# Kernel optimization log

Hardware: AMD Instinct MI355X
Metric: run time of the kernel (lower is better)

Reference implementation:

```python
import jax, jax.numpy as jnp
import numpy as np

B, S, E = 2, 2048, 2048
H, KVH, D = 16, 4, 128
GROUPS = H // KVH
WINDOW = 1024
CAP = 50.0
ROPE_BASE = 10000.0
RMS_EPS = 1e-6
LN_EPS = 1e-5

def setup_inputs() -> dict:
    key = jax.random.key(0)
    ks = jax.random.split(key, 5)
    return {
        "x": jax.random.normal(ks[0], (B, S, E), jnp.float32),
        "Wq": jax.random.normal(ks[1], (E, E), jnp.float32) * (1.0 / np.sqrt(E)),
        "Wk": jax.random.normal(ks[2], (KVH * D, E), jnp.float32) * (1.0 / np.sqrt(E)),
        "Wv": jax.random.normal(ks[3], (KVH * D, E), jnp.float32) * (1.0 / np.sqrt(E)),
        "Wo": jax.random.normal(ks[4], (E, E), jnp.float32) * (1.0 / np.sqrt(E * H)),
        "q_norm_w": jnp.ones((D,), jnp.float32),
        "k_norm_w": jnp.ones((D,), jnp.float32),
        "ln_gamma": jnp.ones((E,), jnp.float32),
        "ln_beta": jnp.zeros((E,), jnp.float32),
    }

def _rmsnorm(t, w):
    # normalize over last (head) dim
    var = jnp.mean(jnp.square(t), axis=-1, keepdims=True)
    return t * jax.lax.rsqrt(var + RMS_EPS) * w

def _rope(t):
    # t: [B, h, S, D]; rotate-half RoPE
    half = D // 2
    inv_freq = 1.0 / (ROPE_BASE ** (jnp.arange(0, D, 2, dtype=jnp.float32) / D))  # [D/2]
    ang = jnp.arange(S, dtype=jnp.float32)[:, None] * inv_freq[None, :]  # [S, D/2]
    cos = jnp.concatenate([jnp.cos(ang), jnp.cos(ang)], axis=-1)  # [S, D]
    sin = jnp.concatenate([jnp.sin(ang), jnp.sin(ang)], axis=-1)
    t1, t2 = t[..., :half], t[..., half:]
    rot = jnp.concatenate([-t2, t1], axis=-1)
    return t * cos + rot * sin

def reference(x, Wq, Wk, Wv, Wo, q_norm_w, k_norm_w, ln_gamma, ln_beta):
    b, s, _ = x.shape
    q = (x @ Wq.T).reshape(b, s, H, D).transpose(0, 2, 1, 3)    # [B,H,S,D]
    k = (x @ Wk.T).reshape(b, s, KVH, D).transpose(0, 2, 1, 3)  # [B,KVH,S,D]
    v = (x @ Wv.T).reshape(b, s, KVH, D).transpose(0, 2, 1, 3)
    # QK-RMSNorm (Gemma/PaLM2 style), then RoPE
    q = _rope(_rmsnorm(q, q_norm_w))
    k = _rope(_rmsnorm(k, k_norm_w))
    # GQA: repeat KV heads to match query heads
    k = jnp.repeat(k, GROUPS, axis=1)  # [B,H,S,D]
    v = jnp.repeat(v, GROUPS, axis=1)
    scores = jnp.einsum('bhqd,bhkd->bhqk', q, k) / jnp.sqrt(jnp.asarray(D, x.dtype))
    # tanh logit softcap (Gemma2)
    scores = CAP * jnp.tanh(scores / CAP)
    # causal + sliding-window mask: attend to j with 0 <= i-j < WINDOW
    i = jnp.arange(s)[:, None]
    j = jnp.arange(s)[None, :]
    mask = (j <= i) & ((i - j) < WINDOW)  # [S,S]
    neg = jnp.finfo(scores.dtype).min
    scores = jnp.where(mask[None, None], scores, neg)
    attn = jax.nn.softmax(scores, axis=-1)
    out = jnp.einsum('bhqk,bhkd->bhqd', attn, v)  # [B,H,S,D]
    out = out.transpose(0, 2, 1, 3).reshape(b, s, E) @ Wo.T
    # residual + LayerNorm (post-norm)
    y = x + out
    mu = jnp.mean(y, axis=-1, keepdims=True)
    var = jnp.var(y, axis=-1, keepdims=True)
    return (y - mu) * jax.lax.rsqrt(var + LN_EPS) * ln_gamma + ln_beta
```

## Files before the change

kernel.cpp:

```cpp
#include <hip/hip_runtime.h>
#include <stdint.h>

typedef __attribute__((ext_vector_type(8))) short short8;
typedef __attribute__((ext_vector_type(4))) float f32x4;
typedef unsigned short u16;
typedef unsigned int u32;

#define NTOK 4096
#define E 2048
#define S 2048
#define NH 16
#define NKVH 4
#define HD 128
#define NQKV 3072

__device__ __forceinline__ float bf2f(u16 u) {
    return __uint_as_float(((u32)u) << 16);
}
__device__ __forceinline__ u16 f2bf(float f) {
    u32 u = __float_as_uint(f);
    u32 r = (u + 0x7fffu + ((u >> 16) & 1u)) >> 16;
    return (u16)r;
}
__device__ __forceinline__ void gload_lds16(const u16* g, u16* l) {
    __builtin_amdgcn_global_load_lds(
        (const __attribute__((address_space(1))) unsigned int*)(g),
        (__attribute__((address_space(3))) unsigned int*)(l), 16, 0, 0);
}

__global__ void cast5(const float* __restrict__ x, const float* __restrict__ wq,
                      const float* __restrict__ wk, const float* __restrict__ wv,
                      const float* __restrict__ wo,
                      u16* __restrict__ xb, u16* __restrict__ wqkvb,
                      u16* __restrict__ wob) {
    int i = blockIdx.x * 256 + threadIdx.x;
    const float* s; u16* d; int rel;
    if (i < 2097152)      { s = x;  d = xb;  rel = i; }
    else if (i < 3145728) { s = wq; d = wqkvb; rel = i - 2097152; }
    else if (i < 3407872) { s = wk; d = wqkvb + 4194304; rel = i - 3145728; }
    else if (i < 3670016) { s = wv; d = wqkvb + 5242880; rel = i - 3407872; }
    else                  { s = wo; d = wob; rel = i - 3670016; }
    float4 v = *(const float4*)(s + (size_t)rel * 4);
    ushort4 o;
    o.x = f2bf(v.x); o.y = f2bf(v.y); o.z = f2bf(v.z); o.w = f2bf(v.w);
    *(ushort4*)(d + (size_t)rel * 4) = o;
}

#define LADDR(row, ko) ((row) * 64 + ((ko) ^ (((row) & 7) << 3)))
#define GSB   __builtin_amdgcn_sched_barrier(0)
#define GBAR  __builtin_amdgcn_s_barrier()
#define LGKM0 do { asm volatile("s_waitcnt lgkmcnt(0)" ::: "memory"); GSB; } while (0)
#define MIDBAR do { GSB; GBAR; LGKM0; } while (0)
#define ENDBAR do { __builtin_amdgcn_s_setprio(0); GSB; GBAR; } while (0)

__device__ __forceinline__ void stage1(u16* lds, const u16* g, int row0,
                                       int kt, int K, int tid) {
    const int rr = tid >> 3;
    const int chunk = (tid & 7) ^ (rr & 7);
    gload_lds16(g + (size_t)(row0 + rr) * K + kt + chunk * 8,
                lds + (row0 + (tid >> 6) * 8) * 64);
}

__global__ __launch_bounds__(512, 2)
void gemm_qkv(const u16* __restrict__ A, const u16* __restrict__ Bt,
              float* __restrict__ C, int M, int N, int K) {
    __shared__ u16 As2[2 * 8192];
    __shared__ u16 Bs2[2 * 24576];
    const int tid = threadIdx.x;
    const int w = tid >> 6, lane = tid & 63;
    const int lr = lane & 15, quad = lane >> 4;
    const int qo = quad * 8;
    const int wr = w >> 2, wc = w & 3;
    const int am = wr * 64;
    const int bn = wc * 96;

    const int nbx = N / 384;
    int wg = blockIdx.x;
    {
        const int nwg = gridDim.x;
        const int q = nwg >> 3, r = nwg & 7;
        const int xcd = wg & 7, loc = wg >> 3;
        wg = (xcd < r ? xcd * (q + 1) : r * (q + 1) + (xcd - r) * q) + loc;
    }
    const int n0 = (wg % nbx) * 384;
    const int m0 = (wg / nbx) * 128;

    const u16* gA = A + (size_t)m0 * K;
    const u16* gB = Bt + (size_t)n0 * K;
    const int nt = K >> 6;

    f32x4 acc[4][6];
#pragma unroll
    for (int mi = 0; mi < 4; mi++)
#pragma unroll
        for (int ni = 0; ni < 6; ni++)
            acc[mi][ni] = (f32x4){0.f, 0.f, 0.f, 0.f};

    short8 af[4][2], bf[6][2];

    stage1(As2, gA, 0, 0, K, tid);
    stage1(As2, gA, 64, 0, K, tid);
#pragma unroll
    for (int r = 0; r < 6; r++) stage1(Bs2, gB, r * 64, 0, K, tid);
    if (nt > 1) {
        stage1(As2 + 8192, gA, 0, 64, K, tid);
        stage1(As2 + 8192, gA, 64, 64, K, tid);
#pragma unroll
        for (int r = 0; r < 4; r++) stage1(Bs2 + 24576, gB, r * 64, 64, K, tid);
        asm volatile("s_waitcnt vmcnt(6)" ::: "memory");
    } else {
        asm volatile("s_waitcnt vmcnt(0)" ::: "memory");
    }
    GSB; GBAR;

    for (int t = 0; t < nt; ++t) {
        const int pb = t & 1;
        u16* Ap = As2 + pb * 8192;
        u16* Bp = Bs2 + pb * 24576;
        u16* Bn = Bs2 + (pb ^ 1) * 24576;
        const int kt1 = (t + 1) << 6, kt2 = (t + 2) << 6;

#pragma unroll
        for (int mi = 0; mi < 4; mi++)
#pragma unroll
            for (int kk = 0; kk < 2; kk++)
                af[mi][kk] = *(const short8*)&Ap[LADDR(am + mi * 16 + lr, kk * 32 + qo)];
#pragma unroll
        for (int ni = 0; ni < 3; ni++)
#pragma unroll
            for (int kk = 0; kk < 2; kk++)
                bf[ni][kk] = *(const short8*)&Bp[LADDR(bn + ni * 16 + lr, kk * 32 + qo)];
        if (t + 1 < nt) {
            stage1(Bn, gB, 256, kt1, K, tid);
            stage1(Bn, gB, 320, kt1, K, tid);
        }
        MIDBAR;
        __builtin_amdgcn_s_setprio(1);
#pragma unroll
        for (int mi = 0; mi < 2; mi++)
#pragma unroll
            for (int ni = 0; ni < 3; ni++)
#pragma unroll
                for (int kk = 0; kk < 2; kk++)
                    acc[mi][ni] = __builtin_amdgcn_mfma_f32_16x16x32_bf16(
                        af[mi][kk], bf[ni][kk], acc[mi][ni], 0, 0, 0);
        ENDBAR;

#pragma unroll
        for (int ni = 3; ni < 6; ni++)
#pragma unroll
            for (int kk = 0; kk < 2; kk++)
                bf[ni][kk] = *(const short8*)&Bp[LADDR(bn + ni * 16 + lr, kk * 32 + qo)];
        if (t + 2 < nt) {
            stage1(Ap, gA, 0, kt2, K, tid);
            stage1(Ap, gA, 64, kt2, K, tid);
        }
        MIDBAR;
        __builtin_amdgcn_s_setprio(1);
#pragma unroll
        for (int mi = 0; mi < 2; mi++)
#pragma unroll
            for (int ni = 3; ni < 6; ni++)
#pragma unroll
                for (int kk = 0; kk < 2; kk++)
                    acc[mi][ni] = __builtin_amdgcn_mfma_f32_16x16x32_bf16(
                        af[mi][kk], bf[ni][kk], acc[mi][ni], 0, 0, 0);
        ENDBAR;

        if (t + 2 < nt) {
#pragma unroll
            for (int r = 0; r < 4; r++) stage1(Bp, gB, r * 64, kt2, K, tid);
        }
        __builtin_amdgcn_s_setprio(1);
#pragma unroll
        for (int mi = 2; mi < 4; mi++)
#pragma unroll
            for (int ni = 0; ni < 6; ni++)
#pragma unroll
                for (int kk = 0; kk < 2; kk++)
                    acc[mi][ni] = __builtin_amdgcn_mfma_f32_16x16x32_bf16(
                        af[mi][kk], bf[ni][kk], acc[mi][ni], 0, 0, 0);
        __builtin_amdgcn_s_setprio(0);
        if (t + 2 >= nt) {
            asm volatile("s_waitcnt vmcnt(0)" ::: "memory");
        } else {
            asm volatile("s_waitcnt vmcnt(6)" ::: "memory");
        }
        GSB; GBAR;
    }

#pragma unroll
    for (int mi = 0; mi < 4; mi++)
#pragma unroll
        for (int ni = 0; ni < 6; ni++) {
            const int row = m0 + am + mi * 16 + quad * 4;
            const int col = n0 + bn + ni * 16 + lr;
            f32x4 v = acc[mi][ni];
            C[(size_t)(row + 0) * N + col] = v[0];
            C[(size_t)(row + 1) * N + col] = v[1];
            C[(size_t)(row + 2) * N + col] = v[2];
            C[(size_t)(row + 3) * N + col] = v[3];
        }
}

__device__ __forceinline__ void stageA(u16* lds, const u16* g, int ldsrow0,
                                       int g0, int g1, int kt, int K, int tid) {
    const int rr = tid >> 3;
    const int chunk = (tid & 7) ^ (rr & 7);
    const int w8 = (tid >> 6) * 8;
    gload_lds16(g + (size_t)(g0 + rr) * K + kt + chunk * 8,
                lds + (ldsrow0 + w8) * 64);
    gload_lds16(g + (size_t)(g1 + rr) * K + kt + chunk * 8,
                lds + (ldsrow0 + 64 + w8) * 64);
}
__device__ __forceinline__ void stageB(u16* lds, const u16* g, int ldsrow0,
                                       int b0, int b1, int kt, int K, int tid) {
    const int rr = tid >> 3;
    const int grow = (rr & 31) | ((rr & 32) << 1);
    const int chunk = (tid & 7) ^ (rr & 7);
    const int w8 = (tid >> 6) * 8;
    gload_lds16(g + (size_t)(b0 + grow) * K + kt + chunk * 8,
                lds + (ldsrow0 + w8) * 64);
    gload_lds16(g + (size_t)(b1 + grow) * K + kt + chunk * 8,
                lds + (ldsrow0 + 64 + w8) * 64);
}

__global__ __launch_bounds__(512, 2)
void gemm8p(const u16* __restrict__ A, const u16* __restrict__ Bt,
            float* __restrict__ C, int M, int N, int K, int ksz, int nsplit) {
    __shared__ u16 As[2 * 16384];
    __shared__ u16 Bs[2 * 16384];
    const int tid = threadIdx.x;
    const int w = tid >> 6, lane = tid & 63;
    const int lr = lane & 15, quad = lane >> 4;
    const int qo = quad * 8;
    const int wm = (w >> 2) * 128, wn = (w & 3) * 64;
    const int wmh = (w >> 2) * 64, wnq = (w & 3) * 32;

    const int nbx = N >> 8;
    int wg = blockIdx.x;
    {
        const int nwg = gridDim.x;
        const int q = nwg >> 3, r = nwg & 7;
        const int xcd = wg & 7, loc = wg >> 3;
        wg = (xcd < r ? xcd * (q + 1) : r * (q + 1) + (xcd - r) * q) + loc;
    }
    int split = 0;
    if (nsplit == 2) { split = wg & 1; wg >>= 1; }
    const int n0 = (wg % nbx) << 8;
    const int m0 = (wg / nbx) << 8;

    const u16* gA = A + (size_t)m0 * K + split * ksz;
    const u16* gB = Bt + (size_t)n0 * K + split * ksz;
    C += (size_t)split * M * N;
    const int nt = ksz >> 6;

    f32x4 acc[8][4];
#pragma unroll
    for (int mi = 0; mi < 8; mi++)
#pragma unroll
        for (int ni = 0; ni < 4; ni++)
            acc[mi][ni] = (f32x4){0.f, 0.f, 0.f, 0.f};

    short8 alo[4][2], ahi[4][2], blo[2][2], bhi[2][2];

    stageA(As, gA, 0, 0, 128, 0, K, tid);
    stageB(Bs, gB, 0, 0, 128, 0, K, tid);
    stageB(Bs, gB, 128, 32, 160, 0, K, tid);
    stageA(As, gA, 128, 64, 192, 0, K, tid);
    if (nt > 1) {
        stageA(As + 16384, gA, 0, 0, 128, 64, K, tid);
        stageB(Bs + 16384, gB, 0, 0, 128, 64, K, tid);
        stageB(Bs + 16384, gB, 128, 32, 160, 64, K, tid);
        asm volatile("s_waitcnt vmcnt(6)" ::: "memory");
    } else {
        asm volatile("s_waitcnt vmcnt(0)" ::: "memory");
    }
    GSB; GBAR;

    for (int t = 0; t < nt; ++t) {
        const int pb = t & 1;
        u16* Ap = As + pb * 16384;
        u16* Bp = Bs + pb * 16384;
        u16* An = As + (pb ^ 1) * 16384;
        const int kt1 = (t + 1) << 6, kt2 = (t + 2) << 6;

#pragma unroll
        for (int mi = 0; mi < 4; mi++)
#pragma unroll
            for (int kk = 0; kk < 2; kk++)
                alo[mi][kk] = *(const short8*)&Ap[LADDR(wmh + mi * 16 + lr, kk * 32 + qo)];
#pragma unroll
        for (int ni = 0; ni < 2; ni++)
#pragma unroll
            for (int kk = 0; kk < 2; kk++)
                blo[ni][kk] = *(const short8*)&Bp[LADDR(wnq + ni * 16 + lr, kk * 32 + qo)];
        if (t + 1 < nt) stageA(An, gA, 128, 64, 192, kt1, K, tid);
        MIDBAR;
        __builtin_amdgcn_s_setprio(1);
#pragma unroll
        for (int mi = 0; mi < 4; mi++)
#pragma unroll
            for (int ni = 0; ni < 2; ni++)
#pragma unroll
                for (int kk = 0; kk < 2; kk++)
                    acc[mi][ni] = __builtin_amdgcn_mfma_f32_16x16x32_bf16(
                        alo[mi][kk], blo[ni][kk], acc[mi][ni], 0, 0, 0);
        ENDBAR;

#pragma unroll
        for (int ni = 0; ni < 2; ni++)
#pragma unroll
            for (int kk = 0; kk < 2; kk++)
                bhi[ni][kk] = *(const short8*)&Bp[LADDR(128 + wnq + ni * 16 + lr, kk * 32 + qo)];
        if (t + 2 < nt) stageA(Ap, gA, 0, 0, 128, kt2, K, tid);
        MIDBAR;
        __builtin_amdgcn_s_setprio(1);
#pragma unroll
        for (int mi = 0; mi < 4; mi++)
#pragma unroll
            for (int ni = 0; ni < 2; ni++)
#pragma unroll
                for (int kk = 0; kk < 2; kk++)
                    acc[mi][ni + 2] = __builtin_amdgcn_mfma_f32_16x16x32_bf16(
                        alo[mi][kk], bhi[ni][kk], acc[mi][ni + 2], 0, 0, 0);
        ENDBAR;

#pragma unroll
        for (int mi = 0; mi < 4; mi++)
#pragma unroll
            for (int kk = 0; kk < 2; kk++)
                ahi[mi][kk] = *(const short8*)&Ap[LADDR(128 + wmh + mi * 16 + lr, kk * 32 + qo)];
        if (t + 2 < nt) stageB(Bp, gB, 0, 0, 128, kt2, K, tid);
        MIDBAR;
        __builtin_amdgcn_s_setprio(1);
#pragma unroll
        for (int mi = 0; mi < 4; mi++)
#pragma unroll
            for (int ni = 0; ni < 2; ni++)
#pragma unroll
                for (int kk = 0; kk < 2; kk++)
                    acc[mi + 4][ni + 2] = __builtin_amdgcn_mfma_f32_16x16x32_bf16(
                        ahi[mi][kk], bhi[ni][kk], acc[mi + 4][ni + 2], 0, 0, 0);
        ENDBAR;

        if (t + 2 < nt) stageB(Bp, gB, 128, 32, 160, kt2, K, tid);
        __builtin_amdgcn_s_setprio(1);
#pragma unroll
        for (int mi = 0; mi < 4; mi++)
#pragma unroll
            for (int ni = 0; ni < 2; ni++)
#pragma unroll
                for (int kk = 0; kk < 2; kk++)
                    acc[mi + 4][ni] = __builtin_amdgcn_mfma_f32_16x16x32_bf16(
                        ahi[mi][kk], blo[ni][kk], acc[mi + 4][ni], 0, 0, 0);
        __builtin_amdgcn_s_setprio(0);
        if (t + 2 >= nt) {
            asm volatile("s_waitcnt vmcnt(0)" ::: "memory");
        } else {
            asm volatile("s_waitcnt vmcnt(6)" ::: "memory");
        }
        GSB; GBAR;
    }

#pragma unroll
    for (int mi = 0; mi < 8; mi++)
#pragma unroll
        for (int ni = 0; ni < 4; ni++) {
            const int row = m0 + wm + mi * 16 + quad * 4;
            const int col = n0 + wn + ni * 16 + lr;
            f32x4 v = acc[mi][ni];
            C[(size_t)(row + 0) * N + col] = v[0];
            C[(size_t)(row + 1) * N + col] = v[1];
            C[(size_t)(row + 2) * N + col] = v[2];
            C[(size_t)(row + 3) * N + col] = v[3];
        }
}

#define LDT 65
#define RMSBLKS 20480
__global__ __launch_bounds__(256)
void prep(const float* __restrict__ qkv,
          const float* __restrict__ qw, const float* __restrict__ kw,
          u16* __restrict__ qdst, u16* __restrict__ kdst, u16* __restrict__ vdst) {
    __shared__ u16 Ts[128 * LDT];
    if (blockIdx.x < RMSBLKS) {
        int p = blockIdx.x * 4 + (threadIdx.x >> 6);
        int lane = threadIdx.x & 63;
        const float* src; const float* w; u16* dst; int HH;
        if (p < NTOK * NH) { src = qkv; w = qw; dst = qdst; HH = NH; }
        else { p -= NTOK * NH; src = qkv + 2048; w = kw; dst = kdst; HH = NKVH; }
        int n = p / HH;
        int h = p - n * HH;
        int b = n >> 11;
        int s = n & 2047;
        const float* row = src + (size_t)n * NQKV + h * HD;
        float t1 = row[lane];
        float t2 = row[lane + 64];
        float ss = t1 * t1 + t2 * t2;
#pragma unroll
        for (int o = 1; o < 64; o <<= 1) ss += __shfl_xor(ss, o);
        float r = rsqrtf(ss * (1.f / 128.f) + 1e-6f);
        float a1 = t1 * r * w[lane];
        float a2 = t2 * r * w[lane + 64];
        float freq = expf(lane * -0.14391156831212787f);
        float ang = (float)s * freq;
        float sn, cs;
        sincosf(ang, &sn, &cs);
        float o1 = a1 * cs - a2 * sn;
        float o2 = a2 * cs + a1 * sn;
        size_t base = (((size_t)(b * HH + h)) * S + s) * HD;
        dst[base + lane] = f2bf(o1);
        dst[base + 64 + lane] = f2bf(o2);
    } else {
        const int idx = blockIdx.x - RMSBLKS;
        const int t = threadIdx.x;
        const int s0 = (idx & 31) * 64;
        const int kh = (idx >> 5) & 3;
        const int b = idx >> 7;
        const float* base = qkv + ((size_t)(b * S + s0)) * NQKV + 2560 + kh * HD;
#pragma unroll
        for (int i = 0; i < 8; i++) {
            int ii = i * 256 + t;
            int r = ii >> 5, c4 = (ii & 31) * 4;
            float4 v = *(const float4*)(base + (size_t)r * NQKV + c4);
            Ts[(c4 + 0) * LDT + r] = f2bf(v.x);
            Ts[(c4 + 1) * LDT + r] = f2bf(v.y);
            Ts[(c4 + 2) * LDT + r] = f2bf(v.z);
            Ts[(c4 + 3) * LDT + r] = f2bf(v.w);
        }
        __syncthreads();
        u16* obase = vdst + ((size_t)(b * NKVH + kh) * HD) * S + s0;
#pragma unroll
        for (int i = 0; i < 4; i++) {
            int ii = i * 256 + t;
            int d = ii >> 3, s8 = (ii & 7) * 8;
            const u16* row = &Ts[d * LDT + s8];
            short8 o;
#pragma unroll
            for (int j = 0; j < 8; j++) o[j] = (short)row[j];
            *(short8*)(obase + (size_t)d * S + s8) = o;
        }
    }
}

#define KSX(key, cb) ((key) * 128 + ((((cb) ^ ((key) & 15))) * 8))
#define VSX(d, cb)   ((d) * 64 + ((((cb) ^ ((d) & 7))) * 8))
#define PSX(row, cb) ((row) * 64 + ((((cb) ^ ((row) & 7))) * 8))
#define QBLK 64

__global__ __launch_bounds__(256, 4)
void attn_mfma(const u16* __restrict__ qa, const u16* __restrict__ ka,
               const u16* __restrict__ vt, u16* __restrict__ out) {
    __shared__ u16 Ks[64 * 128];
    __shared__ u16 Vs[128 * 64];
    __shared__ u16 Ps[64 * 64];
    const int tid = threadIdx.x;
    const int w = tid >> 6, lane = tid & 63;
    const int lr = lane & 15, quad = lane >> 4;

    const int bid = blockIdx.x;
    const int g = bid >> 8, p = bid & 255;
    const int j = p >> 5, hb = p & 31;
    int qt;
    if (g == 0) qt = 31 - j;
    else if (g == 1) qt = 23 - j;
    else if (g == 2) qt = 8 + j;
    else qt = 7 - j;
    const int h = hb >> 1, b = hb & 1;
    const int kh = h >> 2;
    const int q0 = qt * QBLK;
    const int qg0 = q0 + w * 16;

    const float KQK = 0.0051006974f;
    const float KP  = -144.26950408889634f;

    const u16* kbase0 = ka + (((size_t)(b * NKVH + kh)) * S) * HD;
    const u16* vtbase0 = vt + ((size_t)(b * NKVH + kh) * HD) * S;

    short8 qf[4];
    {
        const u16* qrow = qa + (((size_t)(b * NH + h)) * S + qg0 + lr) * HD;
#pragma unroll
        for (int c = 0; c < 4; c++)
            qf[c] = *(const short8*)(qrow + c * 32 + quad * 8);
    }

    f32x4 O[8];
#pragma unroll
    for (int dt = 0; dt < 8; dt++) O[dt] = (f32x4){0.f, 0.f, 0.f, 0.f};
    float l[4] = {0.f, 0.f, 0.f, 0.f};

    const int jt0 = (q0 >= 1024) ? (q0 - 1024) : 0;
    const int jtend = q0;
    const int qmin = qg0, qmax = qg0 + 15;

    for (int jt = jt0; jt <= jtend; jt += 64) {
        const u16* kbase = kbase0 + (size_t)jt * HD;
        const u16* vtbase = vtbase0 + jt;
        __syncthreads();
#pragma unroll
        for (int i = 0; i < 4; i++) {
            int idx = i * 256 + tid;
            int key = idx >> 4, cbk = (idx & 15) ^ (key & 15);
            gload_lds16(kbase + (size_t)key * HD + cbk * 8,
                        &Ks[(i * 256 + w * 64) * 8]);
            int dd = idx >> 3, cbv = (idx & 7) ^ (dd & 7);
            gload_lds16(vtbase + (size_t)dd * S + cbv * 8,
                        &Vs[(i * 256 + w * 64) * 8]);
        }
        __syncthreads();

        u16* Pw = &Ps[w * 16 * 64];
        bool any = false;

#pragma unroll
        for (int kt = 0; kt < 4; kt++) {
            const int keymin = jt + kt * 16;
            bool need = (keymin <= qmax) && (keymin + 15 >= qmin - 1023);
            bool full = (keymin + 15 <= qmin) && (keymin >= qmax - 1023);
            if (need) {
                any = true;
                f32x4 a = (f32x4){0.f, 0.f, 0.f, 0.f};
                __builtin_amdgcn_s_setprio(1);
#pragma unroll
                for (int c = 0; c < 4; c++) {
                    short8 kf = *(const short8*)(&Ks[KSX(kt * 16 + lr, 4 * c + quad)]);
                    a = __builtin_amdgcn_mfma_f32_16x16x32_bf16(qf[c], kf, a, 0, 0, 0);
                }
                __builtin_amdgcn_s_setprio(0);
#pragma unroll
                for (int r = 0; r < 4; r++) {
                    float t = __builtin_amdgcn_exp2f(a[r] * KQK);
                    float p2 = __builtin_amdgcn_exp2f(
                        KP * __builtin_amdgcn_rcpf(t + 1.f));
                    if (!full) {
                        int rel = keymin + lr - (qg0 + quad * 4 + r);
                        bool valid = (rel <= 0) && (rel > -1024);
                        p2 = valid ? p2 : 0.f;
                    }
                    l[r] += p2;
                    Pw[PSX(quad * 4 + r, kt * 2 + (lr >> 3)) + (lr & 7)] =
                        (u16)(__float_as_uint(p2) >> 16);
                }
            } else {
#pragma unroll
                for (int r = 0; r < 4; r++)
                    Pw[PSX(quad * 4 + r, kt * 2 + (lr >> 3)) + (lr & 7)] = 0;
            }
        }

        if (any) {
            __builtin_amdgcn_s_setprio(1);
#pragma unroll
            for (int c2 = 0; c2 < 2; c2++) {
                short8 pf = *(const short8*)(&Pw[PSX(lr, c2 * 4 + quad)]);
#pragma unroll
                for (int dt = 0; dt < 8; dt++) {
                    short8 vf = *(const short8*)(&Vs[VSX(dt * 16 + lr, c2 * 4 + quad)]);
                    O[dt] = __builtin_amdgcn_mfma_f32_16x16x32_bf16(pf, vf, O[dt], 0, 0, 0);
                }
            }
            __builtin_amdgcn_s_setprio(0);
        }
    }

#pragma unroll
    for (int r = 0; r < 4; r++) {
        l[r] += __shfl_xor(l[r], 1);
        l[r] += __shfl_xor(l[r], 2);
        l[r] += __shfl_xor(l[r], 4);
        l[r] += __shfl_xor(l[r], 8);
    }
#pragma unroll
    for (int r = 0; r < 4; r++) {
        float inv = 1.f / l[r];
        u16* orow = out + ((size_t)(b * S + qg0 + quad * 4 + r)) * E + h * HD;
#pragma unroll
        for (int dt = 0; dt < 8; dt++)
            orow[dt * 16 + lr] = f2bf(O[dt][r] * inv);
    }
}

__global__ __launch_bounds__(256)
void ln_kernel(const float* __restrict__ x, const float* __restrict__ pr,
               const float* __restrict__ pr2,
               const float* __restrict__ g, const float* __restrict__ be,
               float* __restrict__ out) {
    int n = blockIdx.x;
    int tid = threadIdx.x;
    const float* xr = x + (size_t)n * E;
    const float* p = pr + (size_t)n * E;
    const float* p2 = pr2 + (size_t)n * E;
    float y[8];
    float s = 0.f, ss = 0.f;
#pragma unroll
    for (int i = 0; i < 2; i++) {
        float4 a = *(const float4*)(xr + tid * 8 + i * 4);
        float4 b = *(const float4*)(p + tid * 8 + i * 4);
        float4 cc = *(const float4*)(p2 + tid * 8 + i * 4);
        float v0 = a.x + b.x + cc.x, v1 = a.y + b.y + cc.y;
        float v2 = a.z + b.z + cc.z, v3 = a.w + b.w + cc.w;
        y[i * 4 + 0] = v0; y[i * 4 + 1] = v1; y[i * 4 + 2] = v2; y[i * 4 + 3] = v3;
        s += v0 + v1 + v2 + v3;
        ss += v0 * v0 + v1 * v1 + v2 * v2 + v3 * v3;
    }
#pragma unroll
    for (int o = 1; o < 64; o <<= 1) {
        s += __shfl_xor(s, o);
        ss += __shfl_xor(ss, o);
    }
    __shared__ float r0[4], r1[4];
    int w = tid >> 6;
    if ((tid & 63) == 0) { r0[w] = s; r1[w] = ss; }
    __syncthreads();
    s = r0[0] + r0[1] + r0[2] + r0[3];
    ss = r1[0] + r1[1] + r1[2] + r1[3];
    float mu = s * (1.f / 2048.f);
    float var = ss * (1.f / 2048.f) - mu * mu;
    float rs = rsqrtf(var + 1e-5f);
    float* orow = out + (size_t)n * E;
#pragma unroll
    for (int i = 0; i < 8; i++) {
        int c = tid * 8 + i;
        orow[c] = (y[i] - mu) * rs * g[c] + be[c];
    }
}

extern "C" void kernel_launch(void* const* d_in, const int* in_sizes, int n_in,
                              void* d_out, int out_size, void* d_ws, size_t ws_size,
                              hipStream_t stream) {
    (void)in_sizes; (void)n_in; (void)out_size; (void)ws_size;
    const float* x   = (const float*)d_in[0];
    const float* Wq  = (const float*)d_in[1];
    const float* Wk  = (const float*)d_in[2];
    const float* Wv  = (const float*)d_in[3];
    const float* Wo  = (const float*)d_in[4];
    const float* qnw = (const float*)d_in[5];
    const float* knw = (const float*)d_in[6];
    const float* lng = (const float*)d_in[7];
    const float* lnb = (const float*)d_in[8];
    float* out = (float*)d_out;

    char* ws = (char*)d_ws;
    size_t off = 0;
    auto alloc = [&](size_t bytes) -> char* {
        char* pp = ws + off;
        off = (off + bytes + 255) & ~(size_t)255;
        return pp;
    };
    u16*  xb     = (u16*)alloc((size_t)NTOK * E * 2);
    u16*  Wqkvb  = (u16*)alloc((size_t)NQKV * E * 2);
    u16*  Wob    = (u16*)alloc((size_t)E * E * 2);
    float* qkvraw= (float*)alloc((size_t)NTOK * NQKV * 4);
    u16*  qaa    = (u16*)alloc((size_t)NTOK * E * 2);
    u16*  kaa    = (u16*)alloc((size_t)NTOK * 512 * 2);
    u16*  vtt    = (u16*)alloc((size_t)NTOK * 512 * 2);
    u16*  attn_o = xb;
    float* proj  = qkvraw;

    cast5<<<dim3(18432), 256, 0, stream>>>(x, Wq, Wk, Wv, Wo, xb, Wqkvb, Wob);

    gemm_qkv<<<dim3(256), 512, 0, stream>>>(xb, Wqkvb, qkvraw, NTOK, NQKV, E);

    prep<<<dim3(RMSBLKS + 256), 256, 0, stream>>>(qkvraw, qnw, knw, qaa, kaa, vtt);

    attn_mfma<<<dim3(1024), 256, 0, stream>>>(qaa, kaa, vtt, attn_o);

    gemm8p<<<dim3((NTOK / 256) * (E / 256) * 2), 512, 0, stream>>>(
        attn_o, Wob, proj, NTOK, E, E, E / 2, 2);

    ln_kernel<<<dim3(NTOK), 256, 0, stream>>>(
        x, proj, proj + (size_t)NTOK * E, lng, lnb, out);
}
```

Baseline: 306.3 us.

## Prefetch next K/V tile into registers to overlap loads with attention compute

The attention loop previously issued direct global-to-LDS loads for each K/V tile and waited on them before computing. It now loads the next tile's K and V into registers right after the barrier, so those loads overlap with the current tile's MFMA work, then stores them to LDS at the top of the next iteration. In exchange it uses more VGPRs (eight int4 values plus index arrays), which may reduce occupancy. It also gives up the direct-to-LDS load path in favour of ordinary vector loads followed by LDS stores.

Result: slower. 422.5 us (+37.9%).

```diff
diff --git a/kernel.cpp b/kernel.cpp
--- a/kernel.cpp
+++ b/kernel.cpp
@@ -495,21 +495,39 @@
     const int jtend = q0;
     const int qmin = qg0, qmax = qg0 + 15;
 
+    int kkey[4], kcb[4], vdd[4], vcb[4];
+#pragma unroll
+    for (int i = 0; i < 4; i++) {
+        int idx = i * 256 + tid;
+        kkey[i] = idx >> 4; kcb[i] = (idx & 15) ^ (kkey[i] & 15);
+        vdd[i] = idx >> 3;  vcb[i] = (idx & 7) ^ (vdd[i] & 7);
+    }
+
+    int4 kreg[4], vreg[4];
+#pragma unroll
+    for (int i = 0; i < 4; i++) {
+        kreg[i] = *(const int4*)(kbase0 + (size_t)(jt0 + kkey[i]) * HD + kcb[i] * 8);
+        vreg[i] = *(const int4*)(vtbase0 + (size_t)vdd[i] * S + jt0 + vcb[i] * 8);
+    }
+
     for (int jt = jt0; jt <= jtend; jt += 64) {
-        const u16* kbase = kbase0 + (size_t)jt * HD;
-        const u16* vtbase = vtbase0 + jt;
         __syncthreads();
 #pragma unroll
         for (int i = 0; i < 4; i++) {
-            int idx = i * 256 + tid;
-            int key = idx >> 4, cbk = (idx & 15) ^ (key & 15);
-            gload_lds16(kbase + (size_t)key * HD + cbk * 8,
-                        &Ks[(i * 256 + w * 64) * 8]);
-            int dd = idx >> 3, cbv = (idx & 7) ^ (dd & 7);
-            gload_lds16(vtbase + (size_t)dd * S + cbv * 8,
-                        &Vs[(i * 256 + w * 64) * 8]);
+            *(int4*)(&Ks[(i * 256 + tid) * 8]) = kreg[i];
+            *(int4*)(&Vs[(i * 256 + tid) * 8]) = vreg[i];
         }
         __syncthreads();
+
+        const bool hasnext = (jt + 64 <= jtend);
+        if (hasnext) {
+            const int jn = jt + 64;
+#pragma unroll
+            for (int i = 0; i < 4; i++) {
+                kreg[i] = *(const int4*)(kbase0 + (size_t)(jn + kkey[i]) * HD + kcb[i] * 8);
+                vreg[i] = *(const int4*)(vtbase0 + (size_t)vdd[i] * S + jn + vcb[i] * 8);
+            }
+        }
 
         u16* Pw = &Ps[w * 16 * 64];
         bool any = false;
```

## Collapse three-phase interleaved GEMM main loop into single load-compute-stage phase

Applied to the files above, without the earlier changes.

Restructures the QKV GEMM main loop: all B fragments are loaded from LDS up front, then one barrier is taken, all 48 MFMAs run in a single block, and the next-next A and B tile prefetches are issued after the compute. This removes two of the intra-iteration barriers and the fine-grained interleaving of global-to-LDS staging with MFMA phases. The trade-off is less overlap of memory staging with compute and higher register pressure from holding all B fragments at once.

Result: no change. 308.8 us (+0.8%).

```diff
diff --git a/kernel.cpp b/kernel.cpp
--- a/kernel.cpp
+++ b/kernel.cpp
@@ -126,7 +126,7 @@
             for (int kk = 0; kk < 2; kk++)
                 af[mi][kk] = *(const short8*)&Ap[LADDR(am + mi * 16 + lr, kk * 32 + qo)];
 #pragma unroll
-        for (int ni = 0; ni < 3; ni++)
+        for (int ni = 0; ni < 6; ni++)
 #pragma unroll
             for (int kk = 0; kk < 2; kk++)
                 bf[ni][kk] = *(const short8*)&Bp[LADDR(bn + ni * 16 + lr, kk * 32 + qo)];
@@ -134,46 +134,10 @@
             stage1(Bn, gB, 256, kt1, K, tid);
             stage1(Bn, gB, 320, kt1, K, tid);
         }
-        MIDBAR;
+        GSB; GBAR; LGKM0;
         __builtin_amdgcn_s_setprio(1);
 #pragma unroll
-        for (int mi = 0; mi < 2; mi++)
-#pragma unroll
-            for (int ni = 0; ni < 3; ni++)
-#pragma unroll
-                for (int kk = 0; kk < 2; kk++)
-                    acc[mi][ni] = __builtin_amdgcn_mfma_f32_16x16x32_bf16(
-                        af[mi][kk], bf[ni][kk], acc[mi][ni], 0, 0, 0);
-        ENDBAR;
-
-#pragma unroll
-        for (int ni = 3; ni < 6; ni++)
-#pragma unroll
-            for (int kk = 0; kk < 2; kk++)
-                bf[ni][kk] = *(const short8*)&Bp[LADDR(bn + ni * 16 + lr, kk * 32 + qo)];
-        if (t + 2 < nt) {
-            stage1(Ap, gA, 0, kt2, K, tid);
-            stage1(Ap, gA, 64, kt2, K, tid);
-        }
-        MIDBAR;
-        __builtin_amdgcn_s_setprio(1);
-#pragma unroll
-        for (int mi = 0; mi < 2; mi++)
-#pragma unroll
-            for (int ni = 3; ni < 6; ni++)
-#pragma unroll
-                for (int kk = 0; kk < 2; kk++)
-                    acc[mi][ni] = __builtin_amdgcn_mfma_f32_16x16x32_bf16(
-                        af[mi][kk], bf[ni][kk], acc[mi][ni], 0, 0, 0);
-        ENDBAR;
-
-        if (t + 2 < nt) {
-#pragma unroll
-            for (int r = 0; r < 4; r++) stage1(Bp, gB, r * 64, kt2, K, tid);
-        }
-        __builtin_amdgcn_s_setprio(1);
-#pragma unroll
-        for (int mi = 2; mi < 4; mi++)
+        for (int mi = 0; mi < 4; mi++)
 #pragma unroll
             for (int ni = 0; ni < 6; ni++)
 #pragma unroll
@@ -181,6 +145,12 @@
                     acc[mi][ni] = __builtin_amdgcn_mfma_f32_16x16x32_bf16(
                         af[mi][kk], bf[ni][kk], acc[mi][ni], 0, 0, 0);
         __builtin_amdgcn_s_setprio(0);
+        if (t + 2 < nt) {
+            stage1(Ap, gA, 0, kt2, K, tid);
+            stage1(Ap, gA, 64, kt2, K, tid);
+#pragma unroll
+            for (int r = 0; r < 4; r++) stage1(Bp, gB, r * 64, kt2, K, tid);
+        }
         if (t + 2 >= nt) {
             asm volatile("s_waitcnt vmcnt(0)" ::: "memory");
         } else {
```
